# Kernel tuning notes

Measured on AMD Instinct MI355X. Metric: run time of the kernel, lower is better.

## Reference

```python
import jax, jax.numpy as jnp
import numpy as np

B, LQ, LKV = 2, 4096, 2048
DQ = DK = DV = 1024
H, DQK, DHV = 16, 64, 64
DOUT = 1024


def _band_mask(span, stride):
    # additive mask: 0 where 0 <= row - col*stride < span, else -inf
    rows = jnp.arange(LQ)[:, None]
    cols = jnp.arange(LKV)[None, :]
    s = rows - cols * stride
    valid = (s >= 0) & (s < span)
    return jnp.where(valid, 0.0, -jnp.inf).astype(jnp.float32)  # [LQ, LKV]


def setup_inputs() -> dict:
    key = jax.random.key(0)
    ks = jax.random.split(key, 7)
    return {
        "q": jax.random.normal(ks[0], (B, LQ, DQ), jnp.float32),
        "k": jax.random.normal(ks[1], (B, LKV, DK), jnp.float32),
        "v": jax.random.normal(ks[2], (B, LKV, DV), jnp.float32),
        # Linear weights stored as [in, out] (x @ W == torch Linear with W.T)
        "Wq": jax.random.normal(ks[3], (DQ, H * DQK), jnp.float32) / np.sqrt(DQ).astype(np.float32),
        "Wk": jax.random.normal(ks[4], (DK, H * DQK), jnp.float32) / np.sqrt(DK).astype(np.float32),
        "Wv": jax.random.normal(ks[5], (DV, H * DHV), jnp.float32) / np.sqrt(DV).astype(np.float32),
        "Wo": jax.random.normal(ks[6], (H * DHV, DOUT), jnp.float32) / np.sqrt(H * DHV).astype(np.float32),
        "span": 16,
        "stride": 2,
    }


def reference(q, k, v, Wq, Wk, Wv, Wo, span, stride):
    mask = _band_mask(span, stride)  # [LQ, LKV]
    Q = (q @ Wq).reshape(B, LQ, H, DQK)   # [B, LQ, H, DQK]
    K = (k @ Wk).reshape(B, LKV, H, DQK)  # [B, LKV, H, DQK]
    V = (v @ Wv).reshape(B, LKV, H, DHV)  # [B, LKV, H, DHV]
    scores = jnp.einsum("bqhd,bkhd->bhqk", Q, K) + mask  # [B, H, LQ, LKV]
    # NOTE: original code softmaxes over dim 2 == the QUERY axis (faithful)
    attn = jax.nn.softmax(scores, axis=2)
    ctx = jnp.einsum("bhqk,bkhd->bqhd", attn, V).reshape(B, LQ, H * DHV)
    return ctx @ Wo  # [B, LQ, DOUT]
```

## Files before the change

kernel.cpp:

```cpp
#include <hip/hip_runtime.h>
#include <cstdint>
#include <cstddef>


typedef _Float16 f16;
typedef _Float16 f16x8 __attribute__((ext_vector_type(8)));
typedef float v4f __attribute__((ext_vector_type(4)));

#define B_  2
#define LQ_ 4096
#define LKV_ 2048
#define DMODEL 1024
#define NH 16
#define HD 64
#define SPAN 16
#define STRIDE 2

#define NQ_ELEMS  ((size_t)B_ * LQ_ * DMODEL)
#define NKV_ELEMS ((size_t)B_ * LKV_ * DMODEL)

#define BAR()   __builtin_amdgcn_s_barrier()
#define LGKM0() asm volatile("s_waitcnt lgkmcnt(0)" ::: "memory")
#define SB0()   __builtin_amdgcn_sched_barrier(0)
#define VM4()   asm volatile("s_waitcnt vmcnt(4)" ::: "memory")
#define VM2()   asm volatile("s_waitcnt vmcnt(2)" ::: "memory")
#define VM0()   asm volatile("s_waitcnt vmcnt(0)" ::: "memory")

__device__ __forceinline__ void async_copy16(const f16* g, f16* l) {
    __builtin_amdgcn_global_load_lds((const __attribute__((address_space(1))) void*)g,
                                     (__attribute__((address_space(3))) void*)l, 16, 0, 0);
}

__global__ __launch_bounds__(256)
void prep_all(const float* __restrict__ W0, const float* __restrict__ W1,
              const float* __restrict__ W2, const float* __restrict__ W3,
              f16* __restrict__ T0, f16* __restrict__ T1,
              f16* __restrict__ T2, f16* __restrict__ T3,
              const float* __restrict__ q, const float* __restrict__ k,
              const float* __restrict__ v,
              f16* __restrict__ qh, f16* __restrict__ kh, f16* __restrict__ vh) {
    const int t = threadIdx.x;
    const int bid = blockIdx.x;
    if (bid < 1024) {
        const int z = bid >> 8, rem = bid & 255;
        const int bx = rem & 15, byy = rem >> 4;
        const float* W;
        f16* Wt;
        switch (z) {
            case 0: W = W0; Wt = T0; break;
            case 1: W = W1; Wt = T1; break;
            case 2: W = W2; Wt = T2; break;
            default: W = W3; Wt = T3; break;
        }
        __shared__ float tile[64][65];
        const int r0 = byy * 64, c0 = bx * 64;
        const int tx = t & 63, ty = t >> 6;
        for (int i = ty; i < 64; i += 4)
            tile[i][tx] = W[(long)(r0 + i) * DMODEL + c0 + tx];
        __syncthreads();
        for (int i = ty; i < 64; i += 4)
            Wt[(long)(c0 + i) * DMODEL + r0 + tx] = (f16)tile[tx][i];
    } else {
        const int cid = bid - 1024;
        const float* src;
        f16* dst;
        size_t base;
        if (cid < 4096)      { src = q; dst = qh; base = (size_t)cid * 2048; }
        else if (cid < 6144) { src = k; dst = kh; base = (size_t)(cid - 4096) * 2048; }
        else                 { src = v; dst = vh; base = (size_t)(cid - 6144) * 2048; }
        const size_t i = base + (size_t)t * 8;
        const float4 lo = *(const float4*)(src + i);
        const float4 hi = *(const float4*)(src + i + 4);
        f16x8 o = {(f16)lo.x, (f16)lo.y, (f16)lo.z, (f16)lo.w,
                   (f16)hi.x, (f16)hi.y, (f16)hi.z, (f16)hi.w};
        *(f16x8*)(dst + i) = o;
    }
}

__device__ __forceinline__ void gemm_qkv_body(const f16* __restrict__ Ah,
                                              const f16* __restrict__ Bt,
                                              f16* __restrict__ C,
                                              int rowTile, int colTile) {
    constexpr int K = DMODEL, N = DMODEL, NT = K / 64;
    __shared__ f16 lds[2 * 32768];

    const int t = threadIdx.x;
    const int lane = t & 63, w = t >> 6;
    const int wm = w >> 2, wn = w & 3;
    const int qrow = lane & 15, quad = lane >> 4;
    const long rowBase = (long)rowTile * 256;
    const long colBase = (long)colTile * 256;

    const int srow = t >> 3, sch = t & 7;
    const int gch = sch ^ (srow & 7);
    const f16* aBase = Ah + (rowBase + srow) * (long)K + gch * 8;
    const f16* bBase = Bt + (colBase + srow) * (long)K + gch * 8;

    v4f acc[8][4] = {};
    f16x8 afr[4][2];
    f16x8 bfr[4][2];

    auto STAGE = [&](int tt2, int op, int half) {
        f16* dst = &lds[(tt2 & 1) * 32768 + op * 16384 + half * 8192 + t * 8];
        const f16* src = (op ? bBase : aBase) + (long)half * 128 * K + tt2 * 64;
        async_copy16(src, dst);
        async_copy16(src + 64 * (long)K, dst + 4096);
    };
    auto DSA = [&](int tt2, int h) {
        const f16* lp = &lds[(tt2 & 1) * 32768];
#pragma unroll
        for (int m4 = 0; m4 < 4; ++m4)
#pragma unroll
            for (int s = 0; s < 2; ++s)
                afr[m4][s] = *(const f16x8*)(lp +
                    (h * 128 + wm * 64 + m4 * 16 + qrow) * 64 +
                    (((s * 4 + quad) ^ (qrow & 7)) * 8));
    };
    auto DSB = [&](int tt2, int h) {
        const f16* lp = &lds[(tt2 & 1) * 32768 + 16384];
#pragma unroll
        for (int n2 = 0; n2 < 2; ++n2)
#pragma unroll
            for (int s = 0; s < 2; ++s)
                bfr[h * 2 + n2][s] = *(const f16x8*)(lp +
                    (h * 128 + wn * 32 + n2 * 16 + qrow) * 64 +
                    (((s * 4 + quad) ^ (qrow & 7)) * 8));
    };
    auto MQ = [&](int ah, int bh) {
        __builtin_amdgcn_s_setprio(1);
#pragma unroll
        for (int s = 0; s < 2; ++s)
#pragma unroll
            for (int m4 = 0; m4 < 4; ++m4)
#pragma unroll
                for (int n2 = 0; n2 < 2; ++n2)
                    acc[ah * 4 + m4][bh * 2 + n2] =
                        __builtin_amdgcn_mfma_f32_16x16x32_f16(
                            afr[m4][s], bfr[bh * 2 + n2][s],
                            acc[ah * 4 + m4][bh * 2 + n2], 0, 0, 0);
        __builtin_amdgcn_s_setprio(0);
    };

    STAGE(0, 0, 0); STAGE(0, 1, 0); STAGE(0, 1, 1); STAGE(0, 0, 1);
    VM0();
    BAR();

#pragma unroll 2
    for (int tt = 0; tt < NT; ++tt) {
        const bool st = (tt + 1 < NT);
        DSA(tt, 0); DSB(tt, 0);
        if (st) STAGE(tt + 1, 0, 0);
        BAR(); LGKM0(); SB0();
        MQ(0, 0);
        if (st) { VM4(); } else { VM2(); }
        BAR();
        DSB(tt, 1);
        if (st) STAGE(tt + 1, 1, 0);
        BAR(); LGKM0(); SB0();
        MQ(0, 1);
        if (st) { VM4(); } else { VM0(); }
        BAR();
        DSA(tt, 1);
        if (st) STAGE(tt + 1, 1, 1);
        BAR(); LGKM0(); SB0();
        MQ(1, 0);
        BAR();
        if (st) STAGE(tt + 1, 0, 1);
        MQ(1, 1);
        if (st) VM4();
        BAR();
    }

#pragma unroll
    for (int m = 0; m < 8; ++m)
#pragma unroll
        for (int n = 0; n < 4; ++n) {
            const int ah = m >> 2, m4 = m & 3;
            const int bh = n >> 1, n2 = n & 1;
            const long col = colBase + bh * 128 + wn * 32 + n2 * 16 + qrow;
#pragma unroll
            for (int r = 0; r < 4; ++r) {
                const long row = rowBase + ah * 128 + wm * 64 + m4 * 16 + quad * 4 + r;
                C[row * (long)N + col] = (f16)acc[m][n][r];
            }
        }
}

__global__ __launch_bounds__(512)
void gemm_qkv(const f16* __restrict__ qf, const f16* __restrict__ kf,
              const f16* __restrict__ vf, const f16* __restrict__ WqT,
              const f16* __restrict__ WkT, const f16* __restrict__ WvT,
              f16* __restrict__ Qh, f16* __restrict__ Kh, f16* __restrict__ Vh) {
    const int id = (blockIdx.x & 7) * 32 + (blockIdx.x >> 3);
    const f16* A; const f16* Bt; f16* C; int rt, ct;
    if (id < 128)      { A = qf; Bt = WqT; C = Qh; rt = id >> 2; ct = id & 3; }
    else if (id < 192) { const int g = id - 128; A = kf; Bt = WkT; C = Kh; rt = g >> 2; ct = g & 3; }
    else               { const int g = id - 192; A = vf; Bt = WvT; C = Vh; rt = g >> 2; ct = g & 3; }
    gemm_qkv_body(A, Bt, C, rt, ct);
}

template <bool OUT_F32>
__device__ __forceinline__ void gemm_body(const f16* __restrict__ Ah,
                                          const f16* __restrict__ Bt,
                                          void* __restrict__ Cv,
                                          int rowTile, int colTile) {
    constexpr int K = DMODEL, N = DMODEL;
    __shared__ f16 As[128 * 64];
    __shared__ f16 Bs[128 * 64];
    const int t = threadIdx.x;
    const int lane = t & 63;
    const int w = t >> 6;
    const int wm = w >> 1, wn = w & 1;
    const long rowBase = (long)rowTile * 128;
    const long colBase = (long)colTile * 128;
    const int qrow = lane & 15;
    const int quad = lane >> 4;

    v4f acc[4][4] = {};

    const int srow = t >> 3;
    const int schunk = t & 7;
    const int gchunk = schunk ^ (srow & 7);
    const f16* aptr = Ah + (rowBase + srow) * (long)K + gchunk * 8;
    const f16* bptr = Bt + (colBase + srow) * (long)K + gchunk * 8;
    f16* lA = &As[srow * 64 + schunk * 8];
    f16* lB = &Bs[srow * 64 + schunk * 8];

    for (int k0 = 0; k0 < K; k0 += 64) {
#pragma unroll
        for (int i = 0; i < 4; ++i)
            async_copy16(bptr + k0 + i * 32 * (long)K, lB + i * 2048);
#pragma unroll
        for (int i = 0; i < 4; ++i)
            async_copy16(aptr + k0 + i * 32 * (long)K, lA + i * 2048);
        __syncthreads();
#pragma unroll
        for (int s = 0; s < 2; ++s) {
            const int xk = (s * 4 + quad) ^ (qrow & 7);
            f16x8 af[4], bf[4];
#pragma unroll
            for (int mt = 0; mt < 4; ++mt)
                af[mt] = *(const f16x8*)(&As[(wm * 64 + mt * 16 + qrow) * 64 + xk * 8]);
#pragma unroll
            for (int nt = 0; nt < 4; ++nt)
                bf[nt] = *(const f16x8*)(&Bs[(wn * 64 + nt * 16 + qrow) * 64 + xk * 8]);
#pragma unroll
            for (int mt = 0; mt < 4; ++mt)
#pragma unroll
                for (int nt = 0; nt < 4; ++nt)
                    acc[mt][nt] = __builtin_amdgcn_mfma_f32_16x16x32_f16(
                        af[mt], bf[nt], acc[mt][nt], 0, 0, 0);
        }
        __syncthreads();
    }

#pragma unroll
    for (int mt = 0; mt < 4; ++mt)
#pragma unroll
        for (int nt = 0; nt < 4; ++nt) {
            const long col = colBase + wn * 64 + nt * 16 + qrow;
#pragma unroll
            for (int r = 0; r < 4; ++r) {
                const long row = rowBase + wm * 64 + mt * 16 + quad * 4 + r;
                if (OUT_F32)
                    ((float*)Cv)[row * (long)N + col] = acc[mt][nt][r];
                else
                    ((f16*)Cv)[row * (long)N + col] = (f16)acc[mt][nt][r];
            }
        }
}

__global__ __launch_bounds__(256, 2)
void gemm_out(const f16* __restrict__ A, const f16* __restrict__ Bt,
              float* __restrict__ C) {
    const int id = blockIdx.x;
    const int xcd = id & 7;
    const int g = id >> 3;
    const int ct = g & 7;
    const int rowIdx = (g >> 3) + xcd * 8;
    gemm_body<true>(A, Bt, (void*)C, rowIdx, ct);
}

__global__ __launch_bounds__(256)
void attn_scores(const f16* __restrict__ Q, const f16* __restrict__ Km,
                 float* __restrict__ attnw) {
    const int c0 = blockIdx.x * 4, b = blockIdx.y;
    const int t = threadIdx.x;
    __shared__ f16 Qs[24 * 1032];
    __shared__ f16 Ks[4 * 1032];

#pragma unroll
    for (int it = 0; it < 12; ++it) {
        const int ch = t + 256 * it;
        const int row = ch >> 7, off = (ch & 127) * 8;
        int qq = 2 * c0 + row;
        if (qq > LQ_ - 1) qq = LQ_ - 1;
        f16x8 x = *(const f16x8*)(Q + (size_t)(b * LQ_ + qq) * DMODEL + off);
        const int h = off >> 6, bb = (off >> 3) & 7;
        *(f16x8*)(&Qs[row * 1032 + h * 64 + ((bb + h) & 7) * 8]) = x;
    }
#pragma unroll
    for (int it = 0; it < 2; ++it) {
        const int ch = t + 256 * it;
        const int row = ch >> 7, off = (ch & 127) * 8;
        f16x8 x = *(const f16x8*)(Km + (size_t)(b * LKV_ + c0 + row) * DMODEL + off);
        const int h = off >> 6, bb = (off >> 3) & 7;
        *(f16x8*)(&Ks[row * 1032 + h * 64 + ((bb + h) & 7) * 8]) = x;
    }
    __syncthreads();

    const int h = t >> 4, j = t & 15;
#pragma unroll
    for (int ci = 0; ci < 4; ++ci) {
        const int c = c0 + ci;
        const int q = STRIDE * c + j;
        const int row = 2 * ci + j;
        float a = 0.f;
#pragma unroll
        for (int bb = 0; bb < 8; ++bb) {
            const int off = h * 64 + ((bb + h) & 7) * 8;
            f16x8 qv = *(const f16x8*)(&Qs[row * 1032 + off]);
            f16x8 kv = *(const f16x8*)(&Ks[ci * 1032 + off]);
#pragma unroll
            for (int u = 0; u < 8; ++u) a += (float)qv[u] * (float)kv[u];
        }
        float s = (q < LQ_) ? a : -1e30f;
        float m = s;
#pragma unroll
        for (int o = 1; o < 16; o <<= 1) m = fmaxf(m, __shfl_xor(m, o, 64));
        float p = (q < LQ_) ? __expf(s - m) : 0.f;
        float sum = p;
#pragma unroll
        for (int o = 1; o < 16; o <<= 1) sum += __shfl_xor(sum, o, 64);
        attnw[(size_t)((b * LKV_ + c) * NH + h) * SPAN + j] = p / sum;
    }
}

__global__ __launch_bounds__(256)
void ctx_gather(const float* __restrict__ attnw, const f16* __restrict__ V,
                f16* __restrict__ ctx) {
    const int q0 = blockIdx.x * 16, b = blockIdx.y;
    const int t = threadIdx.x;
    const int kbase = (q0 >> 1) - 7;
    __shared__ f16 Vs[16 * 1024];
    __shared__ float A_lds[16 * 256];

#pragma unroll
    for (int it = 0; it < 8; ++it) {
        const int ch = t + 256 * it;
        const int row = ch >> 7, off = (ch & 127) * 8;
        int k = kbase + row;
        k = (k < 0) ? 0 : ((k > LKV_ - 1) ? LKV_ - 1 : k);
        *(f16x8*)(&Vs[row * 1024 + off]) =
            *(const f16x8*)(V + (size_t)(b * LKV_ + k) * DMODEL + off);
    }
#pragma unroll
    for (int it = 0; it < 4; ++it) {
        const int ch = t + 256 * it;
        const int row = ch >> 6, off = (ch & 63) * 4;
        int k = kbase + row;
        k = (k < 0) ? 0 : ((k > LKV_ - 1) ? LKV_ - 1 : k);
        *(float4*)(&A_lds[row * 256 + off]) =
            *(const float4*)(attnw + (size_t)(b * LKV_ + k) * 256 + off);
    }
    __syncthreads();

    const int chunk = t & 127;
    const int h = chunk >> 3;
    const int d8 = (chunk & 7) * 8;
    const int qh = t >> 7;
    const int aoff = h * 16 + qh;
    const int kq0 = q0 >> 1;

#pragma unroll
    for (int qp = 0; qp < 8; ++qp) {
        const int q = q0 + qp * 2 + qh;
        float acc[8] = {0.f, 0.f, 0.f, 0.f, 0.f, 0.f, 0.f, 0.f};
#pragma unroll
        for (int i = 0; i < 8; ++i) {
            if (kq0 + qp - i < 0) break;
            const int rr = 7 + qp - i;
            const float wgt = A_lds[rr * 256 + aoff + 2 * i];
            const f16x8 v8 = *(const f16x8*)(&Vs[rr * 1024 + h * 64 + d8]);
#pragma unroll
            for (int u = 0; u < 8; ++u) acc[u] += wgt * (float)v8[u];
        }
        f16x8 o = {(f16)acc[0], (f16)acc[1], (f16)acc[2], (f16)acc[3],
                   (f16)acc[4], (f16)acc[5], (f16)acc[6], (f16)acc[7]};
        *(f16x8*)(ctx + (size_t)(b * LQ_ + q) * DMODEL + h * HD + d8) = o;
    }
}

extern "C" void kernel_launch(void* const* d_in, const int* in_sizes, int n_in,
                              void* d_out, int out_size, void* d_ws, size_t ws_size,
                              hipStream_t stream) {
    const float* q  = (const float*)d_in[0];
    const float* k  = (const float*)d_in[1];
    const float* v  = (const float*)d_in[2];
    const float* Wq = (const float*)d_in[3];
    const float* Wk = (const float*)d_in[4];
    const float* Wv = (const float*)d_in[5];
    const float* Wo = (const float*)d_in[6];
    float* out = (float*)d_out;

    const size_t NW = (size_t)DMODEL * DMODEL;

    char* p = (char*)d_ws;
    f16* WqT = (f16*)p; p += NW * 2;
    f16* WkT = (f16*)p; p += NW * 2;
    f16* WvT = (f16*)p; p += NW * 2;
    f16* WoT = (f16*)p; p += NW * 2;
    f16* Qh  = (f16*)p; p += NQ_ELEMS * 2;
    f16* Kh  = (f16*)p; p += NKV_ELEMS * 2;
    f16* Vh  = (f16*)p; p += NKV_ELEMS * 2;
    f16* qf  = (f16*)p; p += NQ_ELEMS * 2;
    f16* kf  = (f16*)p; p += NKV_ELEMS * 2;
    f16* vf  = (f16*)p; p += NKV_ELEMS * 2;
    f16* ctxh = qf;
    float* attnw = (float*)kf;

    prep_all<<<dim3(9216), 256, 0, stream>>>(Wq, Wk, Wv, Wo, WqT, WkT, WvT, WoT,
                                             q, k, v, qf, kf, vf);

    gemm_qkv<<<dim3(256), 512, 0, stream>>>(qf, kf, vf, WqT, WkT, WvT,
                                            Qh, Kh, Vh);

    attn_scores<<<dim3(LKV_ / 4, B_), 256, 0, stream>>>(Qh, Kh, attnw);

    ctx_gather<<<dim3(LQ_ / 16, B_), 256, 0, stream>>>(attnw, Vh, ctxh);

    gemm_out<<<dim3(512), 256, 0, stream>>>(ctxh, WoT, out);
}
```

Before: 209.1 us.

## Rewrite output GEMM with 256x128 tiles, double-buffered LDS and quarter-step pipelining

Replaces the output projection GEMM, previously 128x128 tiles with 256 threads and a single LDS buffer, with a 512-thread 256x128 tile kernel. The new kernel double-buffers LDS and splits each K-step into four MFMA quarters, interleaving async global-to-LDS loads for the next step with the current math. It uses explicit vmcnt waits, barriers and setprio, which is likely modeled on the gemm_qkv kernel. The aim is to hide global load latency and to raise data reuse per block, at the cost of more LDS per block, fewer blocks (256) and tighter synchronization.

```diff
diff --git a/kernel.cpp b/kernel.cpp
--- a/kernel.cpp
+++ b/kernel.cpp
@@ -23,6 +23,7 @@
 #define LGKM0() asm volatile("s_waitcnt lgkmcnt(0)" ::: "memory")
 #define SB0()   __builtin_amdgcn_sched_barrier(0)
 #define VM4()   asm volatile("s_waitcnt vmcnt(4)" ::: "memory")
+#define VM3()   asm volatile("s_waitcnt vmcnt(3)" ::: "memory")
 #define VM2()   asm volatile("s_waitcnt vmcnt(2)" ::: "memory")
 #define VM0()   asm volatile("s_waitcnt vmcnt(0)" ::: "memory")
 
@@ -199,86 +200,120 @@
     gemm_qkv_body(A, Bt, C, rt, ct);
 }
 
-template <bool OUT_F32>
-__device__ __forceinline__ void gemm_body(const f16* __restrict__ Ah,
-                                          const f16* __restrict__ Bt,
-                                          void* __restrict__ Cv,
-                                          int rowTile, int colTile) {
-    constexpr int K = DMODEL, N = DMODEL;
-    __shared__ f16 As[128 * 64];
-    __shared__ f16 Bs[128 * 64];
+__global__ __launch_bounds__(512)
+void gemm_out(const f16* __restrict__ Ah, const f16* __restrict__ Bt,
+              float* __restrict__ C) {
+    constexpr int K = DMODEL, N = DMODEL, NT = K / 64;
+    __shared__ f16 lds[2 * 24576];
+
+    const int id = (blockIdx.x & 7) * 32 + (blockIdx.x >> 3);
+    const int rt = id >> 3, ct = id & 7;
+
     const int t = threadIdx.x;
-    const int lane = t & 63;
-    const int w = t >> 6;
+    const int lane = t & 63, w = t >> 6;
     const int wm = w >> 1, wn = w & 1;
-    const long rowBase = (long)rowTile * 128;
-    const long colBase = (long)colTile * 128;
-    const int qrow = lane & 15;
-    const int quad = lane >> 4;
+    const int qrow = lane & 15, quad = lane >> 4;
+    const long rowBase = (long)rt * 256;
+    const long colBase = (long)ct * 128;
+
+    const int srow = t >> 3, sch = t & 7;
+    const int gch = sch ^ (srow & 7);
+    const f16* aBase = Ah + (rowBase + srow) * (long)K + gch * 8;
+    const f16* bBase = Bt + (colBase + srow) * (long)K + gch * 8;
 
     v4f acc[4][4] = {};
-
-    const int srow = t >> 3;
-    const int schunk = t & 7;
-    const int gchunk = schunk ^ (srow & 7);
-    const f16* aptr = Ah + (rowBase + srow) * (long)K + gchunk * 8;
-    const f16* bptr = Bt + (colBase + srow) * (long)K + gchunk * 8;
-    f16* lA = &As[srow * 64 + schunk * 8];
-    f16* lB = &Bs[srow * 64 + schunk * 8];
-
-    for (int k0 = 0; k0 < K; k0 += 64) {
-#pragma unroll
-        for (int i = 0; i < 4; ++i)
-            async_copy16(bptr + k0 + i * 32 * (long)K, lB + i * 2048);
-#pragma unroll
-        for (int i = 0; i < 4; ++i)
-            async_copy16(aptr + k0 + i * 32 * (long)K, lA + i * 2048);
-        __syncthreads();
-#pragma unroll
-        for (int s = 0; s < 2; ++s) {
-            const int xk = (s * 4 + quad) ^ (qrow & 7);
-            f16x8 af[4], bf[4];
-#pragma unroll
-            for (int mt = 0; mt < 4; ++mt)
-                af[mt] = *(const f16x8*)(&As[(wm * 64 + mt * 16 + qrow) * 64 + xk * 8]);
-#pragma unroll
-            for (int nt = 0; nt < 4; ++nt)
-                bf[nt] = *(const f16x8*)(&Bs[(wn * 64 + nt * 16 + qrow) * 64 + xk * 8]);
-#pragma unroll
-            for (int mt = 0; mt < 4; ++mt)
-#pragma unroll
-                for (int nt = 0; nt < 4; ++nt)
-                    acc[mt][nt] = __builtin_amdgcn_mfma_f32_16x16x32_f16(
-                        af[mt], bf[nt], acc[mt][nt], 0, 0, 0);
-        }
-        __syncthreads();
-    }
-
-#pragma unroll
-    for (int mt = 0; mt < 4; ++mt)
-#pragma unroll
-        for (int nt = 0; nt < 4; ++nt) {
-            const long col = colBase + wn * 64 + nt * 16 + qrow;
+    f16x8 afr[2][2];
+    f16x8 bfr[4][2];
+
+    auto STAGEA = [&](int tt2, int half) {
+        f16* dst = &lds[(tt2 & 1) * 24576 + half * 8192 + t * 8];
+        const f16* src = aBase + (long)half * 128 * K + tt2 * 64;
+        async_copy16(src, dst);
+        async_copy16(src + 64 * (long)K, dst + 4096);
+    };
+    auto STAGEB = [&](int tt2, int half) {
+        f16* dst = &lds[(tt2 & 1) * 24576 + 16384 + half * 4096 + t * 8];
+        const f16* src = bBase + (long)half * 64 * K + tt2 * 64;
+        async_copy16(src, dst);
+    };
+    auto DSA = [&](int tt2, int h) {
+        const f16* lp = &lds[(tt2 & 1) * 24576];
+#pragma unroll
+        for (int m2 = 0; m2 < 2; ++m2)
+#pragma unroll
+            for (int s = 0; s < 2; ++s)
+                afr[m2][s] = *(const f16x8*)(lp +
+                    (h * 128 + wm * 32 + m2 * 16 + qrow) * 64 +
+                    (((s * 4 + quad) ^ (qrow & 7)) * 8));
+    };
+    auto DSB = [&](int tt2, int h) {
+        const f16* lp = &lds[(tt2 & 1) * 24576 + 16384];
+#pragma unroll
+        for (int n2 = 0; n2 < 2; ++n2)
+#pragma unroll
+            for (int s = 0; s < 2; ++s)
+                bfr[h * 2 + n2][s] = *(const f16x8*)(lp +
+                    (h * 64 + wn * 32 + n2 * 16 + qrow) * 64 +
+                    (((s * 4 + quad) ^ (qrow & 7)) * 8));
+    };
+    auto MQ = [&](int ah, int bh) {
+        __builtin_amdgcn_s_setprio(1);
+#pragma unroll
+        for (int s = 0; s < 2; ++s)
+#pragma unroll
+            for (int m2 = 0; m2 < 2; ++m2)
+#pragma unroll
+                for (int n2 = 0; n2 < 2; ++n2)
+                    acc[ah * 2 + m2][bh * 2 + n2] =
+                        __builtin_amdgcn_mfma_f32_16x16x32_f16(
+                            afr[m2][s], bfr[bh * 2 + n2][s],
+                            acc[ah * 2 + m2][bh * 2 + n2], 0, 0, 0);
+        __builtin_amdgcn_s_setprio(0);
+    };
+
+    STAGEA(0, 0); STAGEB(0, 0); STAGEB(0, 1); STAGEA(0, 1);
+    VM0();
+    BAR();
+
+#pragma unroll 2
+    for (int tt = 0; tt < NT; ++tt) {
+        const bool st = (tt + 1 < NT);
+        DSA(tt, 0); DSB(tt, 0);
+        if (st) STAGEA(tt + 1, 0);
+        BAR(); LGKM0(); SB0();
+        MQ(0, 0);
+        if (st) { VM4(); } else { VM2(); }
+        BAR();
+        DSB(tt, 1);
+        if (st) STAGEB(tt + 1, 0);
+        BAR(); LGKM0(); SB0();
+        MQ(0, 1);
+        if (st) { VM3(); } else { VM0(); }
+        BAR();
+        DSA(tt, 1);
+        if (st) STAGEB(tt + 1, 1);
+        BAR(); LGKM0(); SB0();
+        MQ(1, 0);
+        BAR();
+        if (st) STAGEA(tt + 1, 1);
+        MQ(1, 1);
+        if (st) VM3();
+        BAR();
+    }
+
+#pragma unroll
+    for (int m = 0; m < 4; ++m)
+#pragma unroll
+        for (int n = 0; n < 4; ++n) {
+            const int ah = m >> 1, m2 = m & 1;
+            const int bh = n >> 1, n2 = n & 1;
+            const long col = colBase + bh * 64 + wn * 32 + n2 * 16 + qrow;
 #pragma unroll
             for (int r = 0; r < 4; ++r) {
-                const long row = rowBase + wm * 64 + mt * 16 + quad * 4 + r;
-                if (OUT_F32)
-                    ((float*)Cv)[row * (long)N + col] = acc[mt][nt][r];
-                else
-                    ((f16*)Cv)[row * (long)N + col] = (f16)acc[mt][nt][r];
+                const long row = rowBase + ah * 128 + wm * 32 + m2 * 16 + quad * 4 + r;
+                C[row * (long)N + col] = acc[m][n][r];
             }
         }
-}
-
-__global__ __launch_bounds__(256, 2)
-void gemm_out(const f16* __restrict__ A, const f16* __restrict__ Bt,
-              float* __restrict__ C) {
-    const int id = blockIdx.x;
-    const int xcd = id & 7;
-    const int g = id >> 3;
-    const int ct = g & 7;
-    const int rowIdx = (g >> 3) + xcd * 8;
-    gemm_body<true>(A, Bt, (void*)C, rowIdx, ct);
 }
 
 __global__ __launch_bounds__(256)
@@ -429,5 +464,5 @@
 
     ctx_gather<<<dim3(LQ_ / 16, B_), 256, 0, stream>>>(attnw, Vh, ctxh);
 
-    gemm_out<<<dim3(512), 256, 0, stream>>>(ctxh, WoT, out);
-}
+    gemm_out<<<dim3(256), 512, 0, stream>>>(ctxh, WoT, out);
+}
```

After: 209.4 us. No clear change (+0.1%).
